# Kernel tuning notes

Hardware: AMD Instinct MI355X
Metric: run time of the kernel (lower is better)

The kernel has to match this reference:

```python
import jax, jax.numpy as jnp
import numpy as np

B = 65536      # batch (edges/nodes)
A = 8          # number of attribute node types (len(cfg.node_types))
E = 128        # embedding_size


def setup_inputs() -> dict:
    key = jax.random.key(0)
    k1, k2, k3, k4, k5 = jax.random.split(key, 5)
    image_features = jax.random.normal(k1, (B, E), dtype=jnp.float32)
    edge_attributes = jax.random.normal(k2, (B, A, E), dtype=jnp.float32)
    # nn.Linear(2E -> E): weight [E, 2E], bias [E]
    W_agg = jax.random.normal(k3, (E, 2 * E), dtype=jnp.float32) * (1.0 / np.sqrt(2 * E))
    b_agg = jax.random.normal(k4, (E,), dtype=jnp.float32) * 0.01
    # per-node-type edge-space projection [A, E, E] (kaiming-uniform-like scale)
    proj = jax.random.uniform(k5, (A, E, E), dtype=jnp.float32, minval=-1.0, maxval=1.0) * np.sqrt(6.0 / E)
    return {
        "image_features": image_features,
        "edge_attributes": edge_attributes,
        "W_agg": W_agg,
        "b_agg": b_agg,
        "proj": proj,
    }


def reference(image_features, edge_attributes, W_agg, b_agg, proj):
    # src_embeddings.unsqueeze(1).repeat(1, A, 1) -> broadcast, no copy
    src = jnp.broadcast_to(image_features[:, None, :], edge_attributes.shape)  # [B, A, E]
    x = jnp.concatenate([src, edge_attributes], axis=-1)                       # [B, A, 2E]
    agg = jnp.einsum('bak,ik->bai', x, W_agg) + b_agg                          # Linear(2E->E)
    out = jnp.einsum('bai,aij->baj', agg, proj)                                # per-type matmul
    return out
```

## Files before the change

kernel.cpp:

```cpp
#include <hip/hip_runtime.h>
#include <hip/hip_bf16.h>

typedef __attribute__((ext_vector_type(8))) short short8;
typedef __attribute__((ext_vector_type(4))) float floatx4;

__device__ inline short f2bf(float f) {
  unsigned u = __builtin_bit_cast(unsigned, f);
  unsigned r = u + 0x7fffu + ((u >> 16) & 1u);
  return (short)(r >> 16);
}

__device__ inline short8 cvt8(float4 a, float4 b) {
  short8 r;
  r[0] = f2bf(a.x); r[1] = f2bf(a.y); r[2] = f2bf(a.z); r[3] = f2bf(a.w);
  r[4] = f2bf(b.x); r[5] = f2bf(b.y); r[6] = f2bf(b.z); r[7] = f2bf(b.w);
  return r;
}

__global__ __launch_bounds__(256) void prep_M(
    const float* __restrict__ W, const float* __restrict__ proj,
    const float* __restrict__ bvec, short* __restrict__ Mt,
    float* __restrict__ bias2) {
  int blk = blockIdx.x;
  int a = blk >> 7, j = blk & 127;
  int k = threadIdx.x;
  const float* pj = proj + a * 16384 + j;
  float acc = 0.f;
#pragma unroll 4
  for (int i = 0; i < 128; ++i)
    acc += W[i * 256 + k] * pj[i * 128];
  Mt[a * 32768 + j * 256 + k] = f2bf(acc);
  if (k == 0) {
    float b = 0.f;
    for (int i = 0; i < 128; ++i) b += bvec[i] * pj[i * 128];
    bias2[a * 128 + j] = b;
  }
}

__global__ __launch_bounds__(256, 3) void gemm_main(
    const float* __restrict__ img, const float* __restrict__ edge,
    const short* __restrict__ Mt, const float* __restrict__ bias2,
    float* __restrict__ out) {
  const int tid = threadIdx.x;
  const int a = blockIdx.x & 7;
  const int b0 = (blockIdx.x >> 3) << 7;
  const int wave = tid >> 6, lane = tid & 63;
  const int quad = lane >> 4, l16 = lane & 15;
  const int wm = wave & 1, wn = wave >> 1;

  floatx4 acc[4][4] = {};

  const float* imgB[4];
  const float* edgeB[4];
  const short* mB[4];
#pragma unroll
  for (int mt = 0; mt < 4; ++mt) {
    int row = b0 + wm * 64 + mt * 16 + l16;
    imgB[mt]  = img  + (size_t)row * 128  + quad * 8;
    edgeB[mt] = edge + (size_t)row * 1024 + a * 128 + quad * 8;
  }
  const short* Mta = Mt + a * 32768;
#pragma unroll
  for (int nt = 0; nt < 4; ++nt)
    mB[nt] = Mta + (wn * 64 + nt * 16 + l16) * 256 + quad * 8;

#pragma unroll
  for (int ks = 0; ks < 8; ++ks) {
    float4 v0[4], v1[4];
    short8 bfr[4];
#pragma unroll
    for (int mt = 0; mt < 4; ++mt) {
      const float* s = (ks < 4) ? (imgB[mt] + ks * 32)
                                : (edgeB[mt] + (ks - 4) * 32);
      v0[mt] = *(const float4*)s;
      v1[mt] = *(const float4*)(s + 4);
    }
#pragma unroll
    for (int nt = 0; nt < 4; ++nt)
      bfr[nt] = *(const short8*)(mB[nt] + ks * 32);

    short8 af[4];
#pragma unroll
    for (int mt = 0; mt < 4; ++mt) af[mt] = cvt8(v0[mt], v1[mt]);

#pragma unroll
    for (int mt = 0; mt < 4; ++mt)
#pragma unroll
      for (int nt = 0; nt < 4; ++nt)
        acc[mt][nt] = __builtin_amdgcn_mfma_f32_16x16x32_bf16(
            af[mt], bfr[nt], acc[mt][nt], 0, 0, 0);
  }

  float bias[4];
#pragma unroll
  for (int nt = 0; nt < 4; ++nt)
    bias[nt] = bias2[a * 128 + wn * 64 + nt * 16 + l16];
#pragma unroll
  for (int mt = 0; mt < 4; ++mt)
#pragma unroll
    for (int nt = 0; nt < 4; ++nt) {
      int j = wn * 64 + nt * 16 + l16;
#pragma unroll
      for (int r = 0; r < 4; ++r) {
        int b = b0 + wm * 64 + mt * 16 + quad * 4 + r;
        out[(size_t)b * 1024 + a * 128 + j] = acc[mt][nt][r] + bias[nt];
      }
    }
}

extern "C" void kernel_launch(void* const* d_in, const int* in_sizes, int n_in,
                              void* d_out, int out_size, void* d_ws,
                              size_t ws_size, hipStream_t stream) {
  const float* img  = (const float*)d_in[0];
  const float* edge = (const float*)d_in[1];
  const float* W    = (const float*)d_in[2];
  const float* bv   = (const float*)d_in[3];
  const float* proj = (const float*)d_in[4];
  float* out = (float*)d_out;

  short* Mt = (short*)d_ws;
  float* bias2 = (float*)((char*)d_ws + 8 * 128 * 256 * 2);

  prep_M<<<1024, 256, 0, stream>>>(W, proj, bv, Mt, bias2);
  gemm_main<<<4096, 256, 0, stream>>>(img, edge, Mt, bias2, out);
}
```

Measured before the change: 615.8 us.

## Stage A tile through double-buffered LDS with register prefetch in gemm_main

```diff
diff --git a/kernel.cpp b/kernel.cpp
--- a/kernel.cpp
+++ b/kernel.cpp
@@ -37,10 +37,13 @@
   }
 }
 
-__global__ __launch_bounds__(256, 3) void gemm_main(
+__global__ __launch_bounds__(256) void gemm_main(
     const float* __restrict__ img, const float* __restrict__ edge,
     const short* __restrict__ Mt, const float* __restrict__ bias2,
     float* __restrict__ out) {
+  constexpr int LDA = 40;
+  __shared__ short As[2][128 * LDA];
+
   const int tid = threadIdx.x;
   const int a = blockIdx.x & 7;
   const int b0 = (blockIdx.x >> 3) << 7;
@@ -48,47 +51,65 @@
   const int quad = lane >> 4, l16 = lane & 15;
   const int wm = wave & 1, wn = wave >> 1;
 
+  const int r0 = tid >> 2, c8 = tid & 3;
+  const float* gImg0  = img  + (size_t)(b0 + r0) * 128 + c8 * 8;
+  const float* gImg1  = gImg0 + 64 * 128;
+  const float* gEdge0 = edge + (size_t)(b0 + r0) * 1024 + a * 128 + c8 * 8;
+  const float* gEdge1 = gEdge0 + (size_t)64 * 1024;
+  short* w0p = &As[0][r0 * LDA + c8 * 8];
+  short* w1p = &As[0][(r0 + 64) * LDA + c8 * 8];
+  constexpr int BUFS = 128 * LDA;
+
+  const short* mB[4];
+#pragma unroll
+  for (int nt = 0; nt < 4; ++nt)
+    mB[nt] = Mt + a * 32768 + (wn * 64 + nt * 16 + l16) * 256 + quad * 8;
+
+  int offA[4];
+#pragma unroll
+  for (int mt = 0; mt < 4; ++mt)
+    offA[mt] = (wm * 64 + mt * 16 + l16) * LDA + quad * 8;
+
   floatx4 acc[4][4] = {};
 
-  const float* imgB[4];
-  const float* edgeB[4];
-  const short* mB[4];
-#pragma unroll
-  for (int mt = 0; mt < 4; ++mt) {
-    int row = b0 + wm * 64 + mt * 16 + l16;
-    imgB[mt]  = img  + (size_t)row * 128  + quad * 8;
-    edgeB[mt] = edge + (size_t)row * 1024 + a * 128 + quad * 8;
-  }
-  const short* Mta = Mt + a * 32768;
-#pragma unroll
-  for (int nt = 0; nt < 4; ++nt)
-    mB[nt] = Mta + (wn * 64 + nt * 16 + l16) * 256 + quad * 8;
+  float4 pa0 = *(const float4*)gImg0;
+  float4 pa1 = *(const float4*)(gImg0 + 4);
+  float4 pb0 = *(const float4*)gImg1;
+  float4 pb1 = *(const float4*)(gImg1 + 4);
 
-#pragma unroll
   for (int ks = 0; ks < 8; ++ks) {
-    float4 v0[4], v1[4];
+    const int cur = ks & 1;
+    short8 wa = cvt8(pa0, pa1);
+    short8 wb = cvt8(pb0, pb1);
+    *(short8*)(w0p + cur * BUFS) = wa;
+    *(short8*)(w1p + cur * BUFS) = wb;
+
+    if (ks < 7) {
+      const int nk = ks + 1;
+      const float* s0 = (nk < 4) ? gImg0 + nk * 32 : gEdge0 + (nk - 4) * 32;
+      const float* s1 = (nk < 4) ? gImg1 + nk * 32 : gEdge1 + (nk - 4) * 32;
+      pa0 = *(const float4*)s0;
+      pa1 = *(const float4*)(s0 + 4);
+      pb0 = *(const float4*)s1;
+      pb1 = *(const float4*)(s1 + 4);
+    }
+
+    __syncthreads();
+
     short8 bfr[4];
-#pragma unroll
-    for (int mt = 0; mt < 4; ++mt) {
-      const float* s = (ks < 4) ? (imgB[mt] + ks * 32)
-                                : (edgeB[mt] + (ks - 4) * 32);
-      v0[mt] = *(const float4*)s;
-      v1[mt] = *(const float4*)(s + 4);
-    }
 #pragma unroll
     for (int nt = 0; nt < 4; ++nt)
       bfr[nt] = *(const short8*)(mB[nt] + ks * 32);
 
-    short8 af[4];
+    const short* Ab = As[0] + cur * BUFS;
 #pragma unroll
-    for (int mt = 0; mt < 4; ++mt) af[mt] = cvt8(v0[mt], v1[mt]);
-
-#pragma unroll
-    for (int mt = 0; mt < 4; ++mt)
+    for (int mt = 0; mt < 4; ++mt) {
+      short8 af = *(const short8*)(Ab + offA[mt]);
 #pragma unroll
       for (int nt = 0; nt < 4; ++nt)
         acc[mt][nt] = __builtin_amdgcn_mfma_f32_16x16x32_bf16(
-            af[mt], bfr[nt], acc[mt][nt], 0, 0, 0);
+            af, bfr[nt], acc[mt][nt], 0, 0, 0);
+    }
   }
 
   float bias[4];
```

New measurement: 533.3 us. 1.15x faster.
